# Performance work log

Measured on AMD Instinct MI355X. Metric: run time of the kernel, lower is better.

## Reference

```python
import jax, jax.numpy as jnp
import numpy as np

N_NODES = 10000
N_EDGES = 640000
D = 128  # node / edge / hidden feature dim
EPS = 1e-6


def _relu_mlp(x, params):
    # Dense+relu for all layers except the last (plain Dense)
    for w, b in params[:-1]:
        x = jax.nn.relu(x @ w + b)
    w, b = params[-1]
    return x @ w + b


def _layer_norm(x, scale, bias):
    mean = jnp.mean(x, axis=-1, keepdims=True)
    var = jnp.mean(jnp.square(x - mean), axis=-1, keepdims=True)
    return (x - mean) * jax.lax.rsqrt(var + EPS) * scale + bias


def _he(key, fan_in, fan_out):
    return jax.random.normal(key, (fan_in, fan_out), jnp.float32) * jnp.sqrt(2.0 / fan_in)


def setup_inputs() -> dict:
    key = jax.random.key(0)
    ks = jax.random.split(key, 12)
    nodes = jax.random.normal(ks[0], (N_NODES, D), jnp.float32)
    edges = jax.random.normal(ks[1], (N_EDGES, D), jnp.float32)
    senders = jax.random.randint(ks[2], (N_EDGES,), 0, N_NODES, jnp.int32)
    receivers = jax.random.randint(ks[3], (N_EDGES,), 0, N_NODES, jnp.int32)
    # MessageMLP: [3D -> D -> D -> D]
    msg_w0 = _he(ks[4], 3 * D, D); msg_b0 = jnp.zeros((D,), jnp.float32)
    msg_w1 = _he(ks[5], D, D);     msg_b1 = jnp.zeros((D,), jnp.float32)
    msg_w2 = _he(ks[6], D, D);     msg_b2 = jnp.zeros((D,), jnp.float32)
    # NodeMLP: [2D -> D -> D -> D]
    node_w0 = _he(ks[7], 2 * D, D); node_b0 = jnp.zeros((D,), jnp.float32)
    node_w1 = _he(ks[8], D, D);     node_b1 = jnp.zeros((D,), jnp.float32)
    node_w2 = _he(ks[9], D, D);     node_b2 = jnp.zeros((D,), jnp.float32)
    # W_node residual projection (no bias) + LayerNorm params
    w_node = _he(ks[10], D, D)
    ln_scale = jnp.ones((D,), jnp.float32)
    ln_bias = jnp.zeros((D,), jnp.float32)
    return dict(nodes=nodes, edges=edges, senders=senders, receivers=receivers,
                msg_w0=msg_w0, msg_b0=msg_b0, msg_w1=msg_w1, msg_b1=msg_b1,
                msg_w2=msg_w2, msg_b2=msg_b2,
                node_w0=node_w0, node_b0=node_b0, node_w1=node_w1, node_b1=node_b1,
                node_w2=node_w2, node_b2=node_b2,
                w_node=w_node, ln_scale=ln_scale, ln_bias=ln_bias)


def reference(nodes, edges, senders, receivers,
              msg_w0, msg_b0, msg_w1, msg_b1, msg_w2, msg_b2,
              node_w0, node_b0, node_w1, node_b1, node_w2, node_b2,
              w_node, ln_scale, ln_bias):
    total_nodes = nodes.shape[0]
    # gather sender/receiver features and concat with edge features: [E, 3D]
    msg_in = jnp.concatenate([nodes[senders], nodes[receivers], edges], axis=-1)
    messages = _relu_mlp(msg_in, [(msg_w0, msg_b0), (msg_w1, msg_b1), (msg_w2, msg_b2)])
    # scatter-add messages onto receiving nodes: [N, D]
    aggregated = jax.ops.segment_sum(messages, receivers, num_segments=total_nodes)
    node_in = jnp.concatenate([nodes, aggregated], axis=-1)  # [N, 2D]
    nodes_out = _relu_mlp(node_in, [(node_w0, node_b0), (node_w1, node_b1), (node_w2, node_b2)])
    nodes_new = _layer_norm(nodes @ w_node + nodes_out, ln_scale, ln_bias)
    return nodes_new
```

## Files before the change

### kernel.cpp

```cpp
#include <hip/hip_runtime.h>

#define DF 128
constexpr int N_NODES = 10000;
constexpr int N_EDGES = 640000;

typedef __bf16 bf16x8 __attribute__((ext_vector_type(8)));
typedef float f32x4 __attribute__((ext_vector_type(4)));

__device__ __forceinline__ unsigned short f2bf(float f) {
  unsigned u = __builtin_bit_cast(unsigned, f);
  u += 0x7fffu + ((u >> 16) & 1u);
  return (unsigned short)(u >> 16);
}

__device__ __forceinline__ bf16x8 cvt8(float4 a, float4 b) {
  bf16x8 r;
  r[0] = (__bf16)a.x; r[1] = (__bf16)a.y; r[2] = (__bf16)a.z; r[3] = (__bf16)a.w;
  r[4] = (__bf16)b.x; r[5] = (__bf16)b.y; r[6] = (__bf16)b.z; r[7] = (__bf16)b.w;
  return r;
}

template <bool RELU>
__device__ __forceinline__ void stage_t(char* bufj, const f32x4* accv, int grp, int row16) {
#pragma unroll
  for (int nt = 0; nt < 8; ++nt)
#pragma unroll
    for (int i = 0; i < 4; ++i) {
      const int r = grp * 4 + i;
      const int c = nt * 16 + row16;
      float v = RELU ? fmaxf(accv[nt][i], 0.f) : accv[nt][i];
      *(unsigned short*)(bufj + ((r * 256 + c * 2) ^ ((r & 7) << 4))) = f2bf(v);
    }
}

__device__ __forceinline__ bf16x8 read_a(const char* bufj, int kt, int grp, int row16) {
  return *(const bf16x8*)(bufj + ((row16 * 256 + kt * 64 + grp * 16) ^ ((row16 & 7) << 4)));
}

__global__ void zero_deg(int* __restrict__ deg) {
  int i = blockIdx.x * 256 + threadIdx.x;
  if (i < N_NODES) deg[i] = 0;
}

__global__ void pack_prep(const float* __restrict__ w0, const float* __restrict__ w1,
                          const float* __restrict__ w2, const float* __restrict__ nw0,
                          const float* __restrict__ nw1, const float* __restrict__ nw2,
                          const float* __restrict__ wn, const float* __restrict__ nodes,
                          const int* __restrict__ receivers,
                          unsigned short* __restrict__ dst, unsigned short* __restrict__ nbf,
                          int* __restrict__ deg) {
  int tid = blockIdx.x * blockDim.x + threadIdx.x;
  if (tid < 163840) {
    const float* src; int p;
    if (tid < 49152)       { src = w0;  p = tid; }
    else if (tid < 65536)  { src = w1;  p = tid - 49152; }
    else if (tid < 81920)  { src = w2;  p = tid - 65536; }
    else if (tid < 114688) { src = nw0; p = tid - 81920; }
    else if (tid < 131072) { src = nw1; p = tid - 114688; }
    else if (tid < 147456) { src = nw2; p = tid - 131072; }
    else                   { src = wn;  p = tid - 147456; }
    int i = p & 7, lane = (p >> 3) & 63, tile = p >> 9;
    int nt = tile & 7, kt = tile >> 3;
    int k = kt * 32 + ((lane >> 4) << 3) + i;
    int n = nt * 16 + (lane & 15);
    dst[tid] = f2bf(src[k * 128 + n]);
    return;
  }
  int p = tid - 163840;
  if (p < N_NODES * DF) {
    nbf[p] = f2bf(nodes[p]);
    return;
  }
  p -= N_NODES * DF;
  if (p < N_EDGES) atomicAdd(&deg[receivers[p]], 1);
}

__global__ void scan_kernel(const int* __restrict__ deg, int* __restrict__ cursor) {
  __shared__ int part[1024];
  const int t = threadIdx.x;
  int loc[16];
  int s = 0;
#pragma unroll
  for (int j = 0; j < 16; ++j) {
    int idx = t * 16 + j;
    int v = (idx < N_NODES) ? deg[idx] : 0;
    loc[j] = s;
    s += v;
  }
  part[t] = s;
  __syncthreads();
  for (int off = 1; off < 1024; off <<= 1) {
    int v = part[t];
    int a = (t >= off) ? part[t - off] : 0;
    __syncthreads();
    part[t] = v + a;
    __syncthreads();
  }
  int base = (t > 0) ? part[t - 1] : 0;
#pragma unroll
  for (int j = 0; j < 16; ++j) {
    int idx = t * 16 + j;
    if (idx < N_NODES) cursor[idx] = base + loc[j];
  }
}

__global__ void __launch_bounds__(256) scatter_pq(
    const int* __restrict__ receivers, const int* __restrict__ senders,
    int* __restrict__ cursor, int2* __restrict__ ep, int* __restrict__ rid,
    const unsigned short* __restrict__ nbf, const unsigned short* __restrict__ pw,
    unsigned short* __restrict__ P, unsigned short* __restrict__ Q,
    float* __restrict__ hsum) {
  const int bid = blockIdx.x;
  const int tid = threadIdx.x;
  if (bid < N_EDGES / 256) {
    int e = bid * 256 + tid;
    int r = receivers[e];
    int q = atomicAdd(&cursor[r], 1);
    ep[q] = make_int2(e, senders[e]);
    rid[q] = r;
    return;
  }
  const int pb = bid - N_EDGES / 256;
  const int base_row = pb * 64;
  const int nrows = min(64, N_NODES - base_row);
  {
    float4* hz = (float4*)(hsum + (size_t)base_row * DF);
    for (int c = tid; c < nrows * 32; c += 256) hz[c] = make_float4(0.f, 0.f, 0.f, 0.f);
  }
  const int lane = tid & 63, wave = tid >> 6;
  const int row16 = lane & 15, grp = lane >> 4;
  const int rb = base_row + wave * 16;
  const int rA = min(rb + row16, N_NODES - 1);

  f32x4 aP[8], aQ[8];
#pragma unroll
  for (int nt = 0; nt < 8; ++nt) {
    aP[nt] = (f32x4){0.f, 0.f, 0.f, 0.f};
    aQ[nt] = (f32x4){0.f, 0.f, 0.f, 0.f};
  }
#pragma unroll
  for (int kt = 0; kt < 4; ++kt) {
    bf16x8 af = *(const bf16x8*)(nbf + (size_t)rA * DF + kt * 32 + grp * 8);
#pragma unroll
    for (int nt = 0; nt < 8; ++nt) {
      bf16x8 bwP = *(const bf16x8*)(pw + ((size_t)(kt * 8 + nt) * 64 + lane) * 8);
      bf16x8 bwQ = *(const bf16x8*)(pw + ((size_t)((4 + kt) * 8 + nt) * 64 + lane) * 8);
      aP[nt] = __builtin_amdgcn_mfma_f32_16x16x32_bf16(af, bwP, aP[nt], 0, 0, 0);
      aQ[nt] = __builtin_amdgcn_mfma_f32_16x16x32_bf16(af, bwQ, aQ[nt], 0, 0, 0);
    }
  }
#pragma unroll
  for (int nt = 0; nt < 8; ++nt)
#pragma unroll
    for (int i = 0; i < 4; ++i) {
      const int r = rb + grp * 4 + i;
      if (r < N_NODES) {
        P[(size_t)r * DF + nt * 16 + row16] = f2bf(aP[nt][i]);
        Q[(size_t)r * DF + nt * 16 + row16] = f2bf(aQ[nt][i]);
      }
    }
}

__global__ void __launch_bounds__(512, 2) msg_kernel(
    const float* __restrict__ edges,
    const int2* __restrict__ ep, const int* __restrict__ rid,
    const float* __restrict__ b0, const float* __restrict__ b1,
    const unsigned short* __restrict__ pw,
    const unsigned short* __restrict__ P, const unsigned short* __restrict__ Q,
    float* __restrict__ hsum) {
  __shared__ char lds[131072];
  const int tid = threadIdx.x;
  const int lane = tid & 63, wave = tid >> 6;
  const int row16 = lane & 15, grp = lane >> 4;
  char* hb = lds + 65536 + wave * 8192;

  {
    const float4* src = (const float4*)(pw + 32768);
    float4* dst = (float4*)lds;
    for (int c = tid; c < 4096; c += 512) dst[c] = src[c];
  }

  constexpr int NTILE = N_EDGES / 256;
  int tile = blockIdx.x;

  float4 t0[4][2], t1[4][2];
  int sxc[2], rxc[2];
  int e2_[2], sx2[2], rx2[2];

  {
    const int pb = tile * 256 + wave * 32;
#pragma unroll
    for (int s = 0; s < 2; ++s) {
      int2 es = ep[pb + s * 16 + row16];
      e2_[s] = es.x; sx2[s] = es.y;
      rx2[s] = rid[pb + s * 16 + row16];
    }
#pragma unroll
    for (int k2 = 0; k2 < 4; ++k2) {
      const float* p0 = edges + (size_t)e2_[0] * DF + k2 * 32 + grp * 8;
      const float* p1 = edges + (size_t)e2_[1] * DF + k2 * 32 + grp * 8;
      t0[k2][0] = *(const float4*)p0; t0[k2][1] = *(const float4*)(p0 + 4);
      t1[k2][0] = *(const float4*)p1; t1[k2][1] = *(const float4*)(p1 + 4);
    }
    sxc[0] = sx2[0]; sxc[1] = sx2[1];
    rxc[0] = rx2[0]; rxc[1] = rx2[1];
  }

  __syncthreads();

  for (; tile < NTILE; tile += 256) {
    const int pbase = tile * 256 + wave * 32;
    const bool hasNext = (tile + 256) < NTILE;

    if (hasNext) {
      const int npb = (tile + 256) * 256 + wave * 32;
#pragma unroll
      for (int s = 0; s < 2; ++s) {
        int2 es = ep[npb + s * 16 + row16];
        e2_[s] = es.x; sx2[s] = es.y;
        rx2[s] = rid[npb + s * 16 + row16];
      }
    }

    bf16x8 ebf[2][4];
#pragma unroll
    for (int k2 = 0; k2 < 4; ++k2) {
      ebf[0][k2] = cvt8(t0[k2][0], t0[k2][1]);
      ebf[1][k2] = cvt8(t1[k2][0], t1[k2][1]);
    }

    bf16x8 pqf[2][2][4];
#pragma unroll
    for (int s = 0; s < 2; ++s)
#pragma unroll
      for (int kt = 0; kt < 4; ++kt) {
        pqf[s][0][kt] = *(const bf16x8*)(P + (size_t)sxc[s] * DF + kt * 32 + grp * 8);
        pqf[s][1][kt] = *(const bf16x8*)(Q + (size_t)rxc[s] * DF + kt * 32 + grp * 8);
      }

    f32x4 acc[2][8];
#pragma unroll
    for (int nt = 0; nt < 8; ++nt) {
      float bv = b0[nt * 16 + row16];
      acc[0][nt] = (f32x4){bv, bv, bv, bv};
      acc[1][nt] = (f32x4){bv, bv, bv, bv};
    }
#pragma unroll
    for (int kt = 0; kt < 4; ++kt) {
#pragma unroll
      for (int nt = 0; nt < 8; ++nt) {
        bf16x8 bw = *(const bf16x8*)(lds + ((kt * 8 + nt) * 64 + lane) * 16);
        acc[0][nt] = __builtin_amdgcn_mfma_f32_16x16x32_bf16(ebf[0][kt], bw, acc[0][nt], 0, 0, 0);
        acc[1][nt] = __builtin_amdgcn_mfma_f32_16x16x32_bf16(ebf[1][kt], bw, acc[1][nt], 0, 0, 0);
      }
    }

    if (hasNext) {
#pragma unroll
      for (int k2 = 0; k2 < 4; ++k2) {
        const float* p0 = edges + (size_t)e2_[0] * DF + k2 * 32 + grp * 8;
        const float* p1 = edges + (size_t)e2_[1] * DF + k2 * 32 + grp * 8;
        t0[k2][0] = *(const float4*)p0; t0[k2][1] = *(const float4*)(p0 + 4);
        t1[k2][0] = *(const float4*)p1; t1[k2][1] = *(const float4*)(p1 + 4);
      }
    }

    stage_t<false>(hb, acc[0], grp, row16);
    stage_t<false>(hb + 4096, acc[1], grp, row16);
    asm volatile("s_waitcnt lgkmcnt(0)" ::: "memory");
    __builtin_amdgcn_sched_barrier(0);

#pragma unroll
    for (int nt = 0; nt < 8; ++nt) {
      float bv = b1[nt * 16 + row16];
      acc[0][nt] = (f32x4){bv, bv, bv, bv};
      acc[1][nt] = (f32x4){bv, bv, bv, bv};
    }
#pragma unroll
    for (int kt = 0; kt < 4; ++kt) {
      bf16x8 af[2];
#pragma unroll
      for (int s = 0; s < 2; ++s) {
        bf16x8 raw = read_a(hb + s * 4096, kt, grp, row16);
        bf16x8 pv = pqf[s][0][kt], qv = pqf[s][1][kt];
        bf16x8 h;
#pragma unroll
        for (int j = 0; j < 8; ++j)
          h[j] = (__bf16)fmaxf((float)raw[j] + (float)pv[j] + (float)qv[j], 0.f);
        af[s] = h;
      }
#pragma unroll
      for (int nt = 0; nt < 8; ++nt) {
        bf16x8 bw = *(const bf16x8*)(lds + 32768 + ((kt * 8 + nt) * 64 + lane) * 16);
        acc[0][nt] = __builtin_amdgcn_mfma_f32_16x16x32_bf16(af[0], bw, acc[0][nt], 0, 0, 0);
        acc[1][nt] = __builtin_amdgcn_mfma_f32_16x16x32_bf16(af[1], bw, acc[1][nt], 0, 0, 0);
      }
    }

#pragma unroll
    for (int s = 0; s < 2; ++s) {
      const int q = pbase + s * 16 + grp * 4;
      const int ru = rid[pbase + s * 16];
      const bool uni = (ru == rid[pbase + s * 16 + 15]);
      if (uni) {
#pragma unroll
        for (int nt = 0; nt < 8; ++nt) {
          float t = fmaxf(acc[s][nt][0], 0.f) + fmaxf(acc[s][nt][1], 0.f) +
                    fmaxf(acc[s][nt][2], 0.f) + fmaxf(acc[s][nt][3], 0.f);
          t += __shfl_xor(t, 16);
          t += __shfl_xor(t, 32);
          if (grp == 0)
            unsafeAtomicAdd(hsum + (size_t)ru * DF + nt * 16 + row16, t);
        }
      } else {
        const int ra = rid[q], rb_ = rid[q + 1], rc = rid[q + 2], rd = rid[q + 3];
#pragma unroll
        for (int nt = 0; nt < 8; ++nt) {
          const int col = nt * 16 + row16;
          float run = fmaxf(acc[s][nt][0], 0.f);
          if (rb_ != ra) { unsafeAtomicAdd(hsum + (size_t)ra * DF + col, run); run = 0.f; }
          run += fmaxf(acc[s][nt][1], 0.f);
          if (rc != rb_) { unsafeAtomicAdd(hsum + (size_t)rb_ * DF + col, run); run = 0.f; }
          run += fmaxf(acc[s][nt][2], 0.f);
          if (rd != rc) { unsafeAtomicAdd(hsum + (size_t)rc * DF + col, run); run = 0.f; }
          run += fmaxf(acc[s][nt][3], 0.f);
          unsafeAtomicAdd(hsum + (size_t)rd * DF + col, run);
        }
      }
    }

    sxc[0] = sx2[0]; sxc[1] = sx2[1];
    rxc[0] = rx2[0]; rxc[1] = rx2[1];
    asm volatile("s_waitcnt lgkmcnt(0)" ::: "memory");
    __builtin_amdgcn_sched_barrier(0);
  }
}

__global__ void __launch_bounds__(128) node_kernel(
    const float* __restrict__ nodes, const float* __restrict__ hsum,
    const int* __restrict__ deg, const float* __restrict__ b2,
    const float* __restrict__ nb0, const float* __restrict__ nb1, const float* __restrict__ nb2,
    const unsigned short* __restrict__ pw2,
    const unsigned short* __restrict__ pnw0, const unsigned short* __restrict__ pnw1,
    const unsigned short* __restrict__ pnw2, const unsigned short* __restrict__ pwn,
    const float* __restrict__ ln_s, const float* __restrict__ ln_b,
    float* __restrict__ out) {
  __shared__ char hs[8192];
  const int tid = threadIdx.x, lane = tid & 63, wave = tid >> 6;
  const int row16 = lane & 15, grp = lane >> 4;
  char* hb = hs + wave * 4096;
  const int rb = blockIdx.x * 32 + wave * 16;
  const int rA = min(rb + row16, N_NODES - 1);

  f32x4 accA[8];
  {
    float d0 = (float)deg[min(rb + grp * 4 + 0, N_NODES - 1)];
    float d1 = (float)deg[min(rb + grp * 4 + 1, N_NODES - 1)];
    float d2 = (float)deg[min(rb + grp * 4 + 2, N_NODES - 1)];
    float d3 = (float)deg[min(rb + grp * 4 + 3, N_NODES - 1)];
#pragma unroll
    for (int nt = 0; nt < 8; ++nt) {
      float bc = b2[nt * 16 + row16];
      accA[nt] = (f32x4){d0 * bc, d1 * bc, d2 * bc, d3 * bc};
    }
  }
#pragma unroll
  for (int kt = 0; kt < 4; ++kt) {
    const float* hp = hsum + (size_t)rA * DF + kt * 32 + grp * 8;
    float4 h0 = *(const float4*)hp, h1v = *(const float4*)(hp + 4);
    bf16x8 hi = cvt8(h0, h1v);
    float4 l0, l1;
    l0.x = h0.x - (float)hi[0]; l0.y = h0.y - (float)hi[1];
    l0.z = h0.z - (float)hi[2]; l0.w = h0.w - (float)hi[3];
    l1.x = h1v.x - (float)hi[4]; l1.y = h1v.y - (float)hi[5];
    l1.z = h1v.z - (float)hi[6]; l1.w = h1v.w - (float)hi[7];
    bf16x8 lo = cvt8(l0, l1);
#pragma unroll
    for (int nt = 0; nt < 8; ++nt) {
      bf16x8 bw = *(const bf16x8*)(pw2 + ((size_t)(kt * 8 + nt) * 64 + lane) * 8);
      accA[nt] = __builtin_amdgcn_mfma_f32_16x16x32_bf16(hi, bw, accA[nt], 0, 0, 0);
      accA[nt] = __builtin_amdgcn_mfma_f32_16x16x32_bf16(lo, bw, accA[nt], 0, 0, 0);
    }
  }
  stage_t<false>(hb, accA, grp, row16);
  asm volatile("s_waitcnt lgkmcnt(0)" ::: "memory");
  __builtin_amdgcn_sched_barrier(0);

  f32x4 acc[8];
#pragma unroll
  for (int nt = 0; nt < 8; ++nt) {
    float b = nb0[nt * 16 + row16];
    acc[nt] = (f32x4){b, b, b, b};
  }
#pragma unroll
  for (int kt = 0; kt < 8; ++kt) {
    bf16x8 af;
    if (kt < 4) {
      const float* p = nodes + (size_t)rA * DF + kt * 32 + grp * 8;
      af = cvt8(*(const float4*)p, *(const float4*)(p + 4));
    } else {
      af = read_a(hb, kt - 4, grp, row16);
    }
#pragma unroll
    for (int nt = 0; nt < 8; ++nt) {
      bf16x8 bw = *(const bf16x8*)(pnw0 + ((size_t)(kt * 8 + nt) * 64 + lane) * 8);
      acc[nt] = __builtin_amdgcn_mfma_f32_16x16x32_bf16(af, bw, acc[nt], 0, 0, 0);
    }
  }
  asm volatile("s_waitcnt lgkmcnt(0)" ::: "memory");
  __builtin_amdgcn_sched_barrier(0);
  stage_t<true>(hb, acc, grp, row16);
  asm volatile("s_waitcnt lgkmcnt(0)" ::: "memory");
  __builtin_amdgcn_sched_barrier(0);

  f32x4 acc2[8];
#pragma unroll
  for (int nt = 0; nt < 8; ++nt) {
    float b = nb1[nt * 16 + row16];
    acc2[nt] = (f32x4){b, b, b, b};
  }
#pragma unroll
  for (int kt = 0; kt < 4; ++kt) {
    bf16x8 af = read_a(hb, kt, grp, row16);
#pragma unroll
    for (int nt = 0; nt < 8; ++nt) {
      bf16x8 bw = *(const bf16x8*)(pnw1 + ((size_t)(kt * 8 + nt) * 64 + lane) * 8);
      acc2[nt] = __builtin_amdgcn_mfma_f32_16x16x32_bf16(af, bw, acc2[nt], 0, 0, 0);
    }
  }
  asm volatile("s_waitcnt lgkmcnt(0)" ::: "memory");
  __builtin_amdgcn_sched_barrier(0);
  stage_t<true>(hb, acc2, grp, row16);
  asm volatile("s_waitcnt lgkmcnt(0)" ::: "memory");
  __builtin_amdgcn_sched_barrier(0);

  f32x4 acc3[8];
#pragma unroll
  for (int nt = 0; nt < 8; ++nt) {
    float b = nb2[nt * 16 + row16];
    acc3[nt] = (f32x4){b, b, b, b};
  }
#pragma unroll
  for (int kt = 0; kt < 4; ++kt) {
    bf16x8 af = read_a(hb, kt, grp, row16);
#pragma unroll
    for (int nt = 0; nt < 8; ++nt) {
      bf16x8 bw = *(const bf16x8*)(pnw2 + ((size_t)(kt * 8 + nt) * 64 + lane) * 8);
      acc3[nt] = __builtin_amdgcn_mfma_f32_16x16x32_bf16(af, bw, acc3[nt], 0, 0, 0);
    }
  }
  f32x4 accR[8];
#pragma unroll
  for (int nt = 0; nt < 8; ++nt) accR[nt] = (f32x4){0.f, 0.f, 0.f, 0.f};
#pragma unroll
  for (int kt = 0; kt < 4; ++kt) {
    const float* p = nodes + (size_t)rA * DF + kt * 32 + grp * 8;
    bf16x8 af = cvt8(*(const float4*)p, *(const float4*)(p + 4));
#pragma unroll
    for (int nt = 0; nt < 8; ++nt) {
      bf16x8 bw = *(const bf16x8*)(pwn + ((size_t)(kt * 8 + nt) * 64 + lane) * 8);
      accR[nt] = __builtin_amdgcn_mfma_f32_16x16x32_bf16(af, bw, accR[nt], 0, 0, 0);
    }
  }

  float y[8][4];
#pragma unroll
  for (int nt = 0; nt < 8; ++nt)
#pragma unroll
    for (int i = 0; i < 4; ++i) y[nt][i] = acc3[nt][i] + accR[nt][i];

  float mean[4], rstd[4];
#pragma unroll
  for (int i = 0; i < 4; ++i) {
    float s = 0.f;
#pragma unroll
    for (int nt = 0; nt < 8; ++nt) s += y[nt][i];
    s += __shfl_xor(s, 1); s += __shfl_xor(s, 2);
    s += __shfl_xor(s, 4); s += __shfl_xor(s, 8);
    mean[i] = s * (1.0f / 128.0f);
  }
#pragma unroll
  for (int i = 0; i < 4; ++i) {
    float v = 0.f;
#pragma unroll
    for (int nt = 0; nt < 8; ++nt) {
      float d = y[nt][i] - mean[i];
      v += d * d;
    }
    v += __shfl_xor(v, 1); v += __shfl_xor(v, 2);
    v += __shfl_xor(v, 4); v += __shfl_xor(v, 8);
    rstd[i] = rsqrtf(v * (1.0f / 128.0f) + 1e-6f);
  }
#pragma unroll
  for (int nt = 0; nt < 8; ++nt) {
    const float ls = ln_s[nt * 16 + row16];
    const float lb = ln_b[nt * 16 + row16];
#pragma unroll
    for (int i = 0; i < 4; ++i) {
      const int r = rb + grp * 4 + i;
      if (r < N_NODES)
        out[(size_t)r * DF + nt * 16 + row16] = (y[nt][i] - mean[i]) * rstd[i] * ls + lb;
    }
  }
}

extern "C" void kernel_launch(void* const* d_in, const int* in_sizes, int n_in,
                              void* d_out, int out_size, void* d_ws, size_t ws_size,
                              hipStream_t stream) {
  const float* nodes     = (const float*)d_in[0];
  const float* edges     = (const float*)d_in[1];
  const int*   senders   = (const int*)d_in[2];
  const int*   receivers = (const int*)d_in[3];
  const float* msg_w0 = (const float*)d_in[4];
  const float* msg_b0 = (const float*)d_in[5];
  const float* msg_w1 = (const float*)d_in[6];
  const float* msg_b1 = (const float*)d_in[7];
  const float* msg_w2 = (const float*)d_in[8];
  const float* msg_b2 = (const float*)d_in[9];
  const float* node_w0 = (const float*)d_in[10];
  const float* node_b0 = (const float*)d_in[11];
  const float* node_w1 = (const float*)d_in[12];
  const float* node_b1 = (const float*)d_in[13];
  const float* node_w2 = (const float*)d_in[14];
  const float* node_b2 = (const float*)d_in[15];
  const float* w_node   = (const float*)d_in[16];
  const float* ln_scale = (const float*)d_in[17];
  const float* ln_bias  = (const float*)d_in[18];

  char* ws = (char*)d_ws;
  float* hsum           = (float*)ws;
  unsigned short* pw    = (unsigned short*)(ws + 5120000);
  unsigned short* nbf   = (unsigned short*)(ws + 5447680);
  int* deg              = (int*)(ws + 8007680);
  int* cursor           = (int*)(ws + 8047680);
  int* rid              = (int*)(ws + 8087680);
  int2* ep              = (int2*)(ws + 10647680);
  unsigned short* P     = (unsigned short*)(ws + 15767680);
  unsigned short* Q     = (unsigned short*)(ws + 18327680);

  zero_deg<<<40, 256, 0, stream>>>(deg);

  pack_prep<<<8140, 256, 0, stream>>>(
      msg_w0, msg_w1, msg_w2, node_w0, node_w1, node_w2, w_node, nodes, receivers,
      pw, nbf, deg);

  scan_kernel<<<1, 1024, 0, stream>>>(deg, cursor);

  scatter_pq<<<N_EDGES / 256 + 157, 256, 0, stream>>>(
      receivers, senders, cursor, ep, rid, nbf, pw, P, Q, hsum);

  msg_kernel<<<256, 512, 0, stream>>>(
      edges, ep, rid, msg_b0, msg_b1, pw, P, Q, hsum);

  node_kernel<<<313, 128, 0, stream>>>(nodes, hsum, deg, msg_b2,
                                       node_b0, node_b1, node_b2,
                                       pw + 65536,
                                       pw + 81920, pw + 114688, pw + 131072, pw + 147456,
                                       ln_scale, ln_bias, (float*)d_out);
}
```

Baseline: 325.8 us.

## Pre-sort edge features into receiver order as bf16 during scatter

The scatter kernel now reads each edge's fp32 features coalesced, converts them to bf16 and writes them at the edge's sorted position, and stores only the sender index instead of an (edge, sender) pair. The message kernel then streams contiguous bf16 edge rows in sorted order instead of gathering fp32 rows by edge id, and drops the conversion. The goal is to remove random, full-width fp32 gathers from the MFMA loop and halve the bytes it reads. In exchange it adds an extra scattered bf16 write pass of about 160MB-equivalent work, about 164 MB, in the scatter kernel.

```diff
diff --git a/kernel.cpp b/kernel.cpp
--- a/kernel.cpp
+++ b/kernel.cpp
@@ -104,20 +104,37 @@
   }
 }
 
-__global__ void __launch_bounds__(256) scatter_pq(
+__global__ void __launch_bounds__(256) scatter_copy(
     const int* __restrict__ receivers, const int* __restrict__ senders,
-    int* __restrict__ cursor, int2* __restrict__ ep, int* __restrict__ rid,
+    const float* __restrict__ edges,
+    int* __restrict__ cursor, int* __restrict__ ssend, int* __restrict__ rid,
+    unsigned short* __restrict__ esort,
     const unsigned short* __restrict__ nbf, const unsigned short* __restrict__ pw,
     unsigned short* __restrict__ P, unsigned short* __restrict__ Q,
     float* __restrict__ hsum) {
+  __shared__ int qsh[256];
   const int bid = blockIdx.x;
   const int tid = threadIdx.x;
   if (bid < N_EDGES / 256) {
-    int e = bid * 256 + tid;
-    int r = receivers[e];
-    int q = atomicAdd(&cursor[r], 1);
-    ep[q] = make_int2(e, senders[e]);
+    const int e = bid * 256 + tid;
+    const int r = receivers[e];
+    const int q = atomicAdd(&cursor[r], 1);
+    ssend[q] = senders[e];
     rid[q] = r;
+    qsh[tid] = q;
+    __syncthreads();
+    const int sub = tid & 15;
+    const int g16 = tid >> 4;
+#pragma unroll
+    for (int j = 0; j < 16; ++j) {
+      const int i = g16 + j * 16;
+      const int ee = bid * 256 + i;
+      const int qq = qsh[i];
+      const float* src = edges + (size_t)ee * DF + sub * 8;
+      float4 a = *(const float4*)src;
+      float4 b = *(const float4*)(src + 4);
+      *(bf16x8*)(esort + (size_t)qq * DF + sub * 8) = cvt8(a, b);
+    }
     return;
   }
   const int pb = bid - N_EDGES / 256;
@@ -162,8 +179,8 @@
 }
 
 __global__ void __launch_bounds__(512, 2) msg_kernel(
-    const float* __restrict__ edges,
-    const int2* __restrict__ ep, const int* __restrict__ rid,
+    const unsigned short* __restrict__ esort,
+    const int* __restrict__ ssend, const int* __restrict__ rid,
     const float* __restrict__ b0, const float* __restrict__ b1,
     const unsigned short* __restrict__ pw,
     const unsigned short* __restrict__ P, const unsigned short* __restrict__ Q,
@@ -183,27 +200,20 @@
   constexpr int NTILE = N_EDGES / 256;
   int tile = blockIdx.x;
 
-  float4 t0[4][2], t1[4][2];
-  int sxc[2], rxc[2];
-  int e2_[2], sx2[2], rx2[2];
+  bf16x8 ebf_c[2][4], ebf_n[2][4];
+  int sxc[2], rxc[2], sx2[2], rx2[2];
 
   {
     const int pb = tile * 256 + wave * 32;
 #pragma unroll
     for (int s = 0; s < 2; ++s) {
-      int2 es = ep[pb + s * 16 + row16];
-      e2_[s] = es.x; sx2[s] = es.y;
-      rx2[s] = rid[pb + s * 16 + row16];
-    }
-#pragma unroll
-    for (int k2 = 0; k2 < 4; ++k2) {
-      const float* p0 = edges + (size_t)e2_[0] * DF + k2 * 32 + grp * 8;
-      const float* p1 = edges + (size_t)e2_[1] * DF + k2 * 32 + grp * 8;
-      t0[k2][0] = *(const float4*)p0; t0[k2][1] = *(const float4*)(p0 + 4);
-      t1[k2][0] = *(const float4*)p1; t1[k2][1] = *(const float4*)(p1 + 4);
-    }
-    sxc[0] = sx2[0]; sxc[1] = sx2[1];
-    rxc[0] = rx2[0]; rxc[1] = rx2[1];
+      sxc[s] = ssend[pb + s * 16 + row16];
+      rxc[s] = rid[pb + s * 16 + row16];
+#pragma unroll
+      for (int kt = 0; kt < 4; ++kt)
+        ebf_c[s][kt] = *(const bf16x8*)(esort + (size_t)(pb + s * 16 + row16) * DF +
+                                        kt * 32 + grp * 8);
+    }
   }
 
   __syncthreads();
@@ -216,17 +226,13 @@
       const int npb = (tile + 256) * 256 + wave * 32;
 #pragma unroll
       for (int s = 0; s < 2; ++s) {
-        int2 es = ep[npb + s * 16 + row16];
-        e2_[s] = es.x; sx2[s] = es.y;
+        sx2[s] = ssend[npb + s * 16 + row16];
         rx2[s] = rid[npb + s * 16 + row16];
-      }
-    }
-
-    bf16x8 ebf[2][4];
-#pragma unroll
-    for (int k2 = 0; k2 < 4; ++k2) {
-      ebf[0][k2] = cvt8(t0[k2][0], t0[k2][1]);
-      ebf[1][k2] = cvt8(t1[k2][0], t1[k2][1]);
+#pragma unroll
+        for (int kt = 0; kt < 4; ++kt)
+          ebf_n[s][kt] = *(const bf16x8*)(esort + (size_t)(npb + s * 16 + row16) * DF +
+                                          kt * 32 + grp * 8);
+      }
     }
 
     bf16x8 pqf[2][2][4];
@@ -250,18 +256,8 @@
 #pragma unroll
       for (int nt = 0; nt < 8; ++nt) {
         bf16x8 bw = *(const bf16x8*)(lds + ((kt * 8 + nt) * 64 + lane) * 16);
-        acc[0][nt] = __builtin_amdgcn_mfma_f32_16x16x32_bf16(ebf[0][kt], bw, acc[0][nt], 0, 0, 0);
-        acc[1][nt] = __builtin_amdgcn_mfma_f32_16x16x32_bf16(ebf[1][kt], bw, acc[1][nt], 0, 0, 0);
-      }
-    }
-
-    if (hasNext) {
-#pragma unroll
-      for (int k2 = 0; k2 < 4; ++k2) {
-        const float* p0 = edges + (size_t)e2_[0] * DF + k2 * 32 + grp * 8;
-        const float* p1 = edges + (size_t)e2_[1] * DF + k2 * 32 + grp * 8;
-        t0[k2][0] = *(const float4*)p0; t0[k2][1] = *(const float4*)(p0 + 4);
-        t1[k2][0] = *(const float4*)p1; t1[k2][1] = *(const float4*)(p1 + 4);
+        acc[0][nt] = __builtin_amdgcn_mfma_f32_16x16x32_bf16(ebf_c[0][kt], bw, acc[0][nt], 0, 0, 0);
+        acc[1][nt] = __builtin_amdgcn_mfma_f32_16x16x32_bf16(ebf_c[1][kt], bw, acc[1][nt], 0, 0, 0);
       }
     }
 
@@ -329,8 +325,12 @@
       }
     }
 
-    sxc[0] = sx2[0]; sxc[1] = sx2[1];
-    rxc[0] = rx2[0]; rxc[1] = rx2[1];
+#pragma unroll
+    for (int s = 0; s < 2; ++s) {
+      sxc[s] = sx2[s]; rxc[s] = rx2[s];
+#pragma unroll
+      for (int kt = 0; kt < 4; ++kt) ebf_c[s][kt] = ebf_n[s][kt];
+    }
     asm volatile("s_waitcnt lgkmcnt(0)" ::: "memory");
     __builtin_amdgcn_sched_barrier(0);
   }
@@ -534,9 +534,10 @@
   int* deg              = (int*)(ws + 8007680);
   int* cursor           = (int*)(ws + 8047680);
   int* rid              = (int*)(ws + 8087680);
-  int2* ep              = (int2*)(ws + 10647680);
-  unsigned short* P     = (unsigned short*)(ws + 15767680);
-  unsigned short* Q     = (unsigned short*)(ws + 18327680);
+  int* ssend            = (int*)(ws + 10647680);
+  unsigned short* P     = (unsigned short*)(ws + 13207680);
+  unsigned short* Q     = (unsigned short*)(ws + 15767680);
+  unsigned short* esort = (unsigned short*)(ws + 18327680);
 
   zero_deg<<<40, 256, 0, stream>>>(deg);
 
@@ -546,11 +547,11 @@
 
   scan_kernel<<<1, 1024, 0, stream>>>(deg, cursor);
 
-  scatter_pq<<<N_EDGES / 256 + 157, 256, 0, stream>>>(
-      receivers, senders, cursor, ep, rid, nbf, pw, P, Q, hsum);
+  scatter_copy<<<N_EDGES / 256 + 157, 256, 0, stream>>>(
+      receivers, senders, edges, cursor, ssend, rid, esort, nbf, pw, P, Q, hsum);
 
   msg_kernel<<<256, 512, 0, stream>>>(
-      edges, ep, rid, msg_b0, msg_b1, pw, P, Q, hsum);
+      esort, ssend, rid, msg_b0, msg_b1, pw, P, Q, hsum);
 
   node_kernel<<<313, 128, 0, stream>>>(nodes, hsum, deg, msg_b2,
                                        node_b0, node_b1, node_b2,
```

New measurement: 342.4 us. 5.1% more time.
